# Kernel tuning notes

Hardware: AMD Instinct MI355X
Metric: run time of the kernel (lower is better)

## Reference

```python
import jax, jax.numpy as jnp
import numpy as np

N_OBJ, N_REL = 16384, 32768
HID, POOL = 512, 4096
N_OBJ_CLS, N_REL_CLS = 151, 51


def setup_inputs() -> dict:
    key = jax.random.key(0)
    ks = jax.random.split(key, 12)
    return {
        "edge_ctx": jax.random.normal(ks[0], (N_OBJ, HID), jnp.float32),
        "union_features": jax.random.normal(ks[1], (N_REL, POOL), jnp.float32),
        "pair_idx": jax.random.randint(ks[2], (N_REL, 2), 0, N_OBJ, jnp.int64) if jax.config.jax_enable_x64 else jax.random.randint(ks[2], (N_REL, 2), 0, N_OBJ, jnp.int32),
        "obj_preds": jax.random.randint(ks[3], (N_OBJ,), 0, N_OBJ_CLS, jnp.int32),
        "W_post_emb": jax.random.normal(ks[4], (2 * HID, HID), jnp.float32) * (10.0 / np.sqrt(HID)),
        "b_post_emb": jax.random.normal(ks[5], (2 * HID,), jnp.float32) * 0.01,
        "W_post_cat": jax.random.normal(ks[6], (POOL, 2 * HID), jnp.float32) * (1.0 / np.sqrt(2 * HID)),
        "b_post_cat": jax.random.normal(ks[7], (POOL,), jnp.float32) * 0.01,
        "W_rel": jax.random.normal(ks[8], (N_REL_CLS, POOL), jnp.float32) * (1.0 / np.sqrt(POOL)),
        "b_rel": jax.random.normal(ks[9], (N_REL_CLS,), jnp.float32) * 0.01,
        "freq_bias": jax.random.normal(ks[10], (N_OBJ_CLS, N_OBJ_CLS, N_REL_CLS), jnp.float32),
    }


def reference(edge_ctx, union_features, pair_idx, obj_preds,
              W_post_emb, b_post_emb, W_post_cat, b_post_cat,
              W_rel, b_rel, freq_bias):
    # post_emb: [N_obj, H] -> [N_obj, 2H] -> head/tail reps [N_obj, H]
    edge_rep = edge_ctx @ W_post_emb.T + b_post_emb            # [N_obj, 2H]
    edge_rep = edge_rep.reshape(edge_rep.shape[0], 2, HID)
    head_rep = edge_rep[:, 0]                                  # [N_obj, H]
    tail_rep = edge_rep[:, 1]                                  # [N_obj, H]

    h_idx = pair_idx[:, 0]
    t_idx = pair_idx[:, 1]
    # gather + concat head/tail pair features -> [N_rel, 2H]
    prod_rep = jnp.concatenate([head_rep[h_idx], tail_rep[t_idx]], axis=-1)
    # post_cat linear -> [N_rel, POOL]
    prod_rep = prod_rep @ W_post_cat.T + b_post_cat
    # use_vision, pooling_dim == MLP_HEAD_DIM -> elementwise product
    prod_rep = prod_rep * union_features
    # rel_compress -> [N_rel, num_rel_cls]
    rel_dists = prod_rep @ W_rel.T + b_rel
    # frequency bias lookup indexed by (head class, tail class)
    bias = freq_bias[obj_preds[h_idx], obj_preds[t_idx]]       # [N_rel, num_rel_cls]
    return rel_dists + bias
```

## Files before the change

### kernel.cpp

```cpp
#include <hip/hip_runtime.h>

#define N_OBJ 16384
#define N_REL 32768
#define HID 512
#define POOL 4096
#define NCLS 151
#define NRELCLS 51

#define AS1 __attribute__((address_space(1)))
#define AS3 __attribute__((address_space(3)))

#define LDSSZ 131072

typedef __attribute__((ext_vector_type(8))) short short8;
typedef __attribute__((ext_vector_type(4))) float f32x4;

__device__ __forceinline__ unsigned short f2bf(float x) {
    unsigned u = __float_as_uint(x);
    u += 0x7fff + ((u >> 16) & 1);
    return (unsigned short)(u >> 16);
}

__global__ void cvt_kernel(const float* __restrict__ in, unsigned short* __restrict__ out, long n8) {
    long i = (long)blockIdx.x * blockDim.x + threadIdx.x;
    if (i >= n8) return;
    const float4* p = (const float4*)in;
    float4 a = p[2 * i], b = p[2 * i + 1];
    short8 o;
    o[0] = f2bf(a.x); o[1] = f2bf(a.y); o[2] = f2bf(a.z); o[3] = f2bf(a.w);
    o[4] = f2bf(b.x); o[5] = f2bf(b.y); o[6] = f2bf(b.z); o[7] = f2bf(b.w);
    ((short8*)out)[i] = o;
}

__global__ void cvt_wrel_kernel(const float* __restrict__ W, unsigned short* __restrict__ out) {
    int gid = blockIdx.x * 256 + threadIdx.x;
    int row = gid >> 9;
    int c8 = (gid & 511) << 3;
    short8 o = {};
    if (row < NRELCLS) {
        const float* src = W + (long)row * POOL + c8;
        float4 a = *(const float4*)src, b = *(const float4*)(src + 4);
        o[0] = f2bf(a.x); o[1] = f2bf(a.y); o[2] = f2bf(a.z); o[3] = f2bf(a.w);
        o[4] = f2bf(b.x); o[5] = f2bf(b.y); o[6] = f2bf(b.z); o[7] = f2bf(b.w);
    }
    *(short8*)(out + (long)row * POOL + c8) = o;
}

__device__ __forceinline__ void stage_tile128x64(const unsigned short* __restrict__ src,
                                                 unsigned short* lds,
                                                 int row0, int rowStrideElems, int col0,
                                                 int wave, int lane) {
    const char* s = (const char*)(src + (long)row0 * rowStrideElems + col0);
    long strideB = (long)rowStrideElems * 2;
#pragma unroll
    for (int is = 0; is < 4; ++is) {
        int issue = wave * 4 + is;
        const char* g = s + (long)(issue * 8 + (lane >> 3)) * strideB + (lane & 7) * 16;
        __builtin_amdgcn_global_load_lds((const AS1 void*)g,
                                         (AS3 void*)((char*)lds + issue * 1024),
                                         16, 0, 0);
    }
}

__global__ __launch_bounds__(256) void gemm1_kernel(const unsigned short* __restrict__ A,
                                                    const unsigned short* __restrict__ B,
                                                    const float* __restrict__ bias,
                                                    unsigned short* __restrict__ C) {
    __shared__ __align__(16) unsigned short At[128 * 64];
    __shared__ __align__(16) unsigned short Bt[128 * 64];
    int row0 = blockIdx.x * 128, col0 = blockIdx.y * 128;
    int tid = threadIdx.x, wave = tid >> 6, lane = tid & 63;
    int wr = (wave >> 1) * 64, wc = (wave & 1) * 64;
    int lrow = lane & 15, lko = (lane >> 4) * 8;
    f32x4 acc[4][4] = {};
    for (int kt = 0; kt < HID / 64; ++kt) {
        stage_tile128x64(A, At, row0, HID, kt * 64, wave, lane);
        stage_tile128x64(B, Bt, col0, HID, kt * 64, wave, lane);
        __syncthreads();
#pragma unroll
        for (int ks = 0; ks < 2; ++ks) {
            short8 af[4], bf[4];
#pragma unroll
            for (int mi = 0; mi < 4; ++mi) af[mi] = *(const short8*)(At + (wr + 16 * mi + lrow) * 64 + ks * 32 + lko);
#pragma unroll
            for (int ni = 0; ni < 4; ++ni) bf[ni] = *(const short8*)(Bt + (wc + 16 * ni + lrow) * 64 + ks * 32 + lko);
#pragma unroll
            for (int mi = 0; mi < 4; ++mi)
#pragma unroll
                for (int ni = 0; ni < 4; ++ni)
                    acc[mi][ni] = __builtin_amdgcn_mfma_f32_16x16x32_bf16(af[mi], bf[ni], acc[mi][ni], 0, 0, 0);
        }
        __syncthreads();
    }
#pragma unroll
    for (int mi = 0; mi < 4; ++mi)
#pragma unroll
        for (int ni = 0; ni < 4; ++ni)
#pragma unroll
            for (int i = 0; i < 4; ++i) {
                int r = row0 + wr + 16 * mi + 4 * (lane >> 4) + i;
                int c = col0 + wc + 16 * ni + lrow;
                C[(long)r * 1024 + c] = f2bf(acc[mi][ni][i] + bias[c]);
            }
}

__global__ void init_out_kernel(const int* __restrict__ pair_idx, const int* __restrict__ obj_preds,
                                const float* __restrict__ b_rel, const float* __restrict__ freq_bias,
                                float* __restrict__ out) {
    int r = blockIdx.x * 4 + (threadIdx.x >> 6);
    int lane = threadIdx.x & 63;
    if (lane < NRELCLS) {
        int h = pair_idx[2 * r], t = pair_idx[2 * r + 1];
        long idx = ((long)obj_preds[h] * NCLS + obj_preds[t]) * NRELCLS + lane;
        out[(long)r * NRELCLS + lane] = b_rel[lane] + freq_bias[idx];
    }
}

__device__ __forceinline__ void stage_ab(const char* __restrict__ erepb, const char* __restrict__ Wcb,
                                         char* lds, int s, int t, int col0,
                                         const int* hA, const int* tA, const int* colbA,
                                         const int* obaseA, int w, int lane) {
    int kb = t * 64;
#pragma unroll
    for (int i = 0; i < 2; ++i) {
        int idx = (kb < 1024) ? hA[i] : tA[i];
        __builtin_amdgcn_global_load_lds((const AS1 void*)(erepb + (long)idx * 2048 + kb + colbA[i]),
                                         (AS3 void*)(lds + s * 16384 + obaseA[i]), 16, 0, 0);
        int o = obaseA[i] + lane * 16;
        int row = o >> 6, cin = o & 63;
        int c = cin ^ ((row & 3) << 4);
        __builtin_amdgcn_global_load_lds((const AS1 void*)(Wcb + (long)(col0 + row) * 2048 + kb + c),
                                         (AS3 void*)(lds + 65536 + s * 16384 + obaseA[i]), 16, 0, 0);
    }
}

__device__ __forceinline__ void kstep(const char* lds, int s, int wr, int wc, int lrow, int lcb,
                                      f32x4 acc[8][4]) {
    const char* A = lds + s * 16384;
    const char* B = lds + 65536 + s * 16384;
    short8 bfr[4];
#pragma unroll
    for (int ni = 0; ni < 4; ++ni) {
        int r = wc + 16 * ni + lrow;
        bfr[ni] = *(const short8*)(B + r * 64 + (lcb ^ ((r & 3) << 4)));
    }
    __builtin_amdgcn_s_setprio(1);
#pragma unroll
    for (int mi = 0; mi < 8; ++mi) {
        int r = wr + 16 * mi + lrow;
        short8 a = *(const short8*)(A + r * 64 + (lcb ^ ((r & 3) << 4)));
#pragma unroll
        for (int ni = 0; ni < 4; ++ni)
            acc[mi][ni] = __builtin_amdgcn_mfma_f32_16x16x32_bf16(a, bfr[ni], acc[mi][ni], 0, 0, 0);
    }
    __builtin_amdgcn_s_setprio(0);
}

__global__ __launch_bounds__(512, 1) void fused_kernel(
    const unsigned short* __restrict__ erep,
    const unsigned short* __restrict__ Wcat,
    const unsigned short* __restrict__ Wrelp,
    const float* __restrict__ unionf,
    const float* __restrict__ bcat,
    const int* __restrict__ pair_idx,
    float* __restrict__ out) {
    __shared__ __align__(16) char lds[LDSSZ];
    int bid = blockIdx.x;
    int xcd = bid & 7, j = bid >> 3;
    int panel = (xcd << 1) | (j >> 7);
    int row0 = (j & 127) * 256, col0 = panel * 256;
    int tid = threadIdx.x, w = tid >> 6, lane = tid & 63;
    int wr = (w >> 2) * 128, wc = (w & 3) * 64;
    int lrow = lane & 15, lcb = (lane >> 4) * 16;
    const char* erepb = (const char*)erep;
    const char* Wcb = (const char*)Wcat;
    f32x4 acc2[8][4] = {};

    int hA[2], tA[2], colbA[2], obaseA[2];
#pragma unroll
    for (int i = 0; i < 2; ++i) {
        obaseA[i] = i * 8192 + w * 1024;
        int o = obaseA[i] + lane * 16;
        int arow = o >> 6, cin = o & 63;
        colbA[i] = cin ^ ((arow & 3) << 4);
        hA[i] = pair_idx[2 * (row0 + arow)];
        tA[i] = pair_idx[2 * (row0 + arow) + 1];
    }

    stage_ab(erepb, Wcb, lds, 0, 0, col0, hA, tA, colbA, obaseA, w, lane);
    stage_ab(erepb, Wcb, lds, 1, 1, col0, hA, tA, colbA, obaseA, w, lane);
    stage_ab(erepb, Wcb, lds, 2, 2, col0, hA, tA, colbA, obaseA, w, lane);

    for (int t = 0; t < 30; ++t) {
        asm volatile("s_waitcnt vmcnt(8)" ::: "memory");
        __builtin_amdgcn_s_barrier();
        __builtin_amdgcn_sched_barrier(0);
        if (t < 29) stage_ab(erepb, Wcb, lds, (t + 3) & 3, t + 3, col0, hA, tA, colbA, obaseA, w, lane);
        kstep(lds, t & 3, wr, wc, lrow, lcb, acc2);
    }
    asm volatile("s_waitcnt vmcnt(4)" ::: "memory");
    __builtin_amdgcn_s_barrier();
    __builtin_amdgcn_sched_barrier(0);
    kstep(lds, 30 & 3, wr, wc, lrow, lcb, acc2);
    asm volatile("s_waitcnt vmcnt(0)" ::: "memory");
    __builtin_amdgcn_s_barrier();
    __builtin_amdgcn_sched_barrier(0);
    kstep(lds, 31 & 3, wr, wc, lrow, lcb, acc2);

    asm volatile("s_waitcnt lgkmcnt(0)" ::: "memory");
    __builtin_amdgcn_sched_barrier(0);
    __builtin_amdgcn_s_barrier();
    __builtin_amdgcn_sched_barrier(0);

    {
        float bcv[4];
#pragma unroll
        for (int ni = 0; ni < 4; ++ni) bcv[ni] = bcat[col0 + wc + 16 * ni + lrow];
#pragma unroll
        for (int mi = 0; mi < 8; ++mi)
#pragma unroll
            for (int ni = 0; ni < 4; ++ni) {
                int pcol = wc + 16 * ni + lrow;
#pragma unroll
                for (int i = 0; i < 4; ++i) {
                    int prow = wr + 16 * mi + 4 * (lane >> 4) + i;
                    float u = __builtin_nontemporal_load(
                        &unionf[(long)(row0 + prow) * 4096 + col0 + pcol]);
                    *(unsigned short*)(lds + prow * 512 + ((pcol * 2) ^ ((prow & 7) << 4)))
                        = f2bf((acc2[mi][ni][i] + bcv[ni]) * u);
                }
            }
    }
    asm volatile("s_waitcnt lgkmcnt(0)" ::: "memory");
    __builtin_amdgcn_sched_barrier(0);
    __builtin_amdgcn_s_barrier();
    __builtin_amdgcn_sched_barrier(0);

    f32x4 acc3[2][4] = {};
    const char* Wrb = (const char*)Wrelp;
#pragma unroll
    for (int ks = 0; ks < 8; ++ks) {
        int cb2 = ks * 64 + lcb;
        short8 wb[4], pa[2];
#pragma unroll
        for (int ni = 0; ni < 4; ++ni) {
            int r2 = 16 * ni + lrow;
            wb[ni] = *(const short8*)(Wrb + (long)r2 * 8192 + col0 * 2 + cb2);
        }
#pragma unroll
        for (int mi = 0; mi < 2; ++mi) {
            int r2 = w * 32 + 16 * mi + lrow;
            pa[mi] = *(const short8*)(lds + r2 * 512 + (cb2 ^ ((r2 & 7) << 4)));
        }
#pragma unroll
        for (int mi = 0; mi < 2; ++mi)
#pragma unroll
            for (int ni = 0; ni < 4; ++ni)
                acc3[mi][ni] = __builtin_amdgcn_mfma_f32_16x16x32_bf16(pa[mi], wb[ni], acc3[mi][ni], 0, 0, 0);
    }
#pragma unroll
    for (int mi = 0; mi < 2; ++mi)
#pragma unroll
        for (int ni = 0; ni < 4; ++ni)
#pragma unroll
            for (int i = 0; i < 4; ++i) {
                int r = row0 + w * 32 + 16 * mi + 4 * (lane >> 4) + i;
                int cc = 16 * ni + lrow;
                if (cc < NRELCLS) atomicAdd(out + (long)r * NRELCLS + cc, acc3[mi][ni][i]);
            }
}

extern "C" void kernel_launch(void* const* d_in, const int* in_sizes, int n_in,
                              void* d_out, int out_size, void* d_ws, size_t ws_size,
                              hipStream_t stream) {
    const float* edge_ctx  = (const float*)d_in[0];
    const float* unionf    = (const float*)d_in[1];
    const int*   pair_idx  = (const int*)d_in[2];
    const int*   obj_preds = (const int*)d_in[3];
    const float* W_emb     = (const float*)d_in[4];
    const float* b_emb     = (const float*)d_in[5];
    const float* W_cat     = (const float*)d_in[6];
    const float* b_cat     = (const float*)d_in[7];
    const float* W_rel     = (const float*)d_in[8];
    const float* b_rel     = (const float*)d_in[9];
    const float* freq_bias = (const float*)d_in[10];
    float* out = (float*)d_out;

    char* ws = (char*)d_ws;
    unsigned short* ecb   = (unsigned short*)ws; ws += (size_t)N_OBJ * HID * 2;
    unsigned short* Wembb = (unsigned short*)ws; ws += (size_t)1024 * HID * 2;
    unsigned short* Wcatb = (unsigned short*)ws; ws += (size_t)POOL * 1024 * 2;
    unsigned short* Wrelb = (unsigned short*)ws; ws += (size_t)64 * POOL * 2;
    unsigned short* erep  = (unsigned short*)ws; ws += (size_t)N_OBJ * 1024 * 2;

    cvt_kernel<<<4096, 256, 0, stream>>>(edge_ctx, ecb, (long)N_OBJ * HID / 8);
    cvt_kernel<<<256, 256, 0, stream>>>(W_emb, Wembb, (long)1024 * HID / 8);
    cvt_kernel<<<2048, 256, 0, stream>>>(W_cat, Wcatb, (long)POOL * 1024 / 8);
    cvt_wrel_kernel<<<128, 256, 0, stream>>>(W_rel, Wrelb);
    gemm1_kernel<<<dim3(128, 8), 256, 0, stream>>>(ecb, Wembb, b_emb, erep);
    init_out_kernel<<<8192, 256, 0, stream>>>(pair_idx, obj_preds, b_rel, freq_bias, out);
    fused_kernel<<<2048, 512, 0, stream>>>(erep, Wcatb, Wrelb, unionf, b_cat, pair_idx, out);
}
```

Before: 552.0 us.

## Switch GEMM mainloop to double-buffered 128-wide K tiles with interleaved staging

Changes the post_cat GEMM mainloop from a 4-stage ring of 64-byte K slices to 2 LDS buffers of 128-byte K slices, cutting the iteration count from 32 to 16. The loads for the next tile are issued in two halves, interleaved with four sub-phases of MFMA work, and the swizzle is widened to 8 rows. The aim is fewer barriers per unit of compute and finer overlap of loads with MFMAs. The cost is a shallower prefetch depth and extra barriers inside each iteration, which may expose load latency for the gathered rows.

```diff
diff --git a/kernel.cpp b/kernel.cpp
--- a/kernel.cpp
+++ b/kernel.cpp
@@ -116,43 +116,52 @@
     }
 }
 
-__device__ __forceinline__ void stage_ab(const char* __restrict__ erepb, const char* __restrict__ Wcb,
-                                         char* lds, int s, int t, int col0,
-                                         const int* hA, const int* tA, const int* colbA,
-                                         const int* obaseA, int w, int lane) {
-    int kb = t * 64;
-#pragma unroll
-    for (int i = 0; i < 2; ++i) {
-        int idx = (kb < 1024) ? hA[i] : tA[i];
+__device__ __forceinline__ void stage_half(const char* __restrict__ erepb, const char* __restrict__ Wcb,
+                                           char* lds, int slot, int t, int i0, int col0,
+                                           const int* hA, const int* tA,
+                                           const int* arowA, const int* colbA, int w) {
+    int kb = t * 128;
+    int head = (kb < 1024);
+#pragma unroll
+    for (int i = i0; i < i0 + 2; ++i) {
+        int obase = i * 8192 + w * 1024;
+        int idx = head ? hA[i] : tA[i];
         __builtin_amdgcn_global_load_lds((const AS1 void*)(erepb + (long)idx * 2048 + kb + colbA[i]),
-                                         (AS3 void*)(lds + s * 16384 + obaseA[i]), 16, 0, 0);
-        int o = obaseA[i] + lane * 16;
-        int row = o >> 6, cin = o & 63;
-        int c = cin ^ ((row & 3) << 4);
-        __builtin_amdgcn_global_load_lds((const AS1 void*)(Wcb + (long)(col0 + row) * 2048 + kb + c),
-                                         (AS3 void*)(lds + 65536 + s * 16384 + obaseA[i]), 16, 0, 0);
-    }
-}
-
-__device__ __forceinline__ void kstep(const char* lds, int s, int wr, int wc, int lrow, int lcb,
-                                      f32x4 acc[8][4]) {
-    const char* A = lds + s * 16384;
-    const char* B = lds + 65536 + s * 16384;
-    short8 bfr[4];
-#pragma unroll
-    for (int ni = 0; ni < 4; ++ni) {
-        int r = wc + 16 * ni + lrow;
-        bfr[ni] = *(const short8*)(B + r * 64 + (lcb ^ ((r & 3) << 4)));
-    }
+                                         (AS3 void*)(lds + slot * 32768 + obase), 16, 0, 0);
+        __builtin_amdgcn_global_load_lds((const AS1 void*)(Wcb + (long)(col0 + arowA[i]) * 2048 + kb + colbA[i]),
+                                         (AS3 void*)(lds + 65536 + slot * 32768 + obase), 16, 0, 0);
+    }
+}
+
+__device__ __forceinline__ void read_bfrags(const char* B, int wc, int lrow, int lcb, short8 bF[4][2]) {
+#pragma unroll
+    for (int ni = 0; ni < 4; ++ni)
+#pragma unroll
+        for (int ks = 0; ks < 2; ++ks) {
+            int r = wc + 16 * ni + lrow;
+            bF[ni][ks] = *(const short8*)(B + r * 128 + ((ks * 64 + lcb) ^ ((r & 7) << 4)));
+        }
+}
+
+__device__ __forceinline__ void read_afrags(const char* A, int p, int wr, int lrow, int lcb, short8 aF[2][2]) {
+#pragma unroll
+    for (int m = 0; m < 2; ++m)
+#pragma unroll
+        for (int ks = 0; ks < 2; ++ks) {
+            int r = wr + 16 * (2 * p + m) + lrow;
+            aF[m][ks] = *(const short8*)(A + r * 128 + ((ks * 64 + lcb) ^ ((r & 7) << 4)));
+        }
+}
+
+__device__ __forceinline__ void mfma16(int p, short8 aF[2][2], short8 bF[4][2], f32x4 acc[8][4]) {
     __builtin_amdgcn_s_setprio(1);
 #pragma unroll
-    for (int mi = 0; mi < 8; ++mi) {
-        int r = wr + 16 * mi + lrow;
-        short8 a = *(const short8*)(A + r * 64 + (lcb ^ ((r & 3) << 4)));
+    for (int m = 0; m < 2; ++m)
 #pragma unroll
         for (int ni = 0; ni < 4; ++ni)
-            acc[mi][ni] = __builtin_amdgcn_mfma_f32_16x16x32_bf16(a, bfr[ni], acc[mi][ni], 0, 0, 0);
-    }
+#pragma unroll
+            for (int ks = 0; ks < 2; ++ks)
+                acc[2 * p + m][ni] = __builtin_amdgcn_mfma_f32_16x16x32_bf16(aF[m][ks], bF[ni][ks], acc[2 * p + m][ni], 0, 0, 0);
     __builtin_amdgcn_s_setprio(0);
 }
 
@@ -176,36 +185,52 @@
     const char* Wcb = (const char*)Wcat;
     f32x4 acc2[8][4] = {};
 
-    int hA[2], tA[2], colbA[2], obaseA[2];
-#pragma unroll
-    for (int i = 0; i < 2; ++i) {
-        obaseA[i] = i * 8192 + w * 1024;
-        int o = obaseA[i] + lane * 16;
-        int arow = o >> 6, cin = o & 63;
-        colbA[i] = cin ^ ((arow & 3) << 4);
-        hA[i] = pair_idx[2 * (row0 + arow)];
-        tA[i] = pair_idx[2 * (row0 + arow) + 1];
-    }
-
-    stage_ab(erepb, Wcb, lds, 0, 0, col0, hA, tA, colbA, obaseA, w, lane);
-    stage_ab(erepb, Wcb, lds, 1, 1, col0, hA, tA, colbA, obaseA, w, lane);
-    stage_ab(erepb, Wcb, lds, 2, 2, col0, hA, tA, colbA, obaseA, w, lane);
-
-    for (int t = 0; t < 30; ++t) {
-        asm volatile("s_waitcnt vmcnt(8)" ::: "memory");
-        __builtin_amdgcn_s_barrier();
-        __builtin_amdgcn_sched_barrier(0);
-        if (t < 29) stage_ab(erepb, Wcb, lds, (t + 3) & 3, t + 3, col0, hA, tA, colbA, obaseA, w, lane);
-        kstep(lds, t & 3, wr, wc, lrow, lcb, acc2);
-    }
-    asm volatile("s_waitcnt vmcnt(4)" ::: "memory");
-    __builtin_amdgcn_s_barrier();
-    __builtin_amdgcn_sched_barrier(0);
-    kstep(lds, 30 & 3, wr, wc, lrow, lcb, acc2);
-    asm volatile("s_waitcnt vmcnt(0)" ::: "memory");
-    __builtin_amdgcn_s_barrier();
-    __builtin_amdgcn_sched_barrier(0);
-    kstep(lds, 31 & 3, wr, wc, lrow, lcb, acc2);
+    int hA[4], tA[4], arowA[4], colbA[4];
+#pragma unroll
+    for (int i = 0; i < 4; ++i) {
+        int o = i * 8192 + w * 1024 + lane * 16;
+        int ar = o >> 7, cin = o & 127;
+        arowA[i] = ar;
+        colbA[i] = cin ^ ((ar & 7) << 4);
+        hA[i] = pair_idx[2 * (row0 + ar)];
+        tA[i] = pair_idx[2 * (row0 + ar) + 1];
+    }
+
+    stage_half(erepb, Wcb, lds, 0, 0, 0, col0, hA, tA, arowA, colbA, w);
+    stage_half(erepb, Wcb, lds, 0, 0, 2, col0, hA, tA, arowA, colbA, w);
+
+    for (int t = 0; t < 16; ++t) {
+        const char* A = lds + (t & 1) * 32768;
+        const char* B = lds + 65536 + (t & 1) * 32768;
+        int sn = (t + 1) & 1;
+        short8 bF[4][2];
+#pragma unroll
+        for (int p = 0; p < 4; ++p) {
+            short8 aF[2][2];
+            if (p == 0) {
+                if (t < 15) {
+                    stage_half(erepb, Wcb, lds, sn, t + 1, 0, col0, hA, tA, arowA, colbA, w);
+                    asm volatile("s_waitcnt vmcnt(4)" ::: "memory");
+                } else {
+                    asm volatile("s_waitcnt vmcnt(0)" ::: "memory");
+                }
+                __builtin_amdgcn_s_barrier();
+                __builtin_amdgcn_sched_barrier(0);
+                read_bfrags(B, wc, lrow, lcb, bF);
+                read_afrags(A, 0, wr, lrow, lcb, aF);
+            } else {
+                read_afrags(A, p, wr, lrow, lcb, aF);
+                if (p == 2 && t < 15)
+                    stage_half(erepb, Wcb, lds, sn, t + 1, 2, col0, hA, tA, arowA, colbA, w);
+                __builtin_amdgcn_s_barrier();
+                __builtin_amdgcn_sched_barrier(0);
+            }
+            asm volatile("s_waitcnt lgkmcnt(0)" ::: "memory");
+            __builtin_amdgcn_sched_barrier(0);
+            mfma16(p, aF, bF, acc2);
+            __builtin_amdgcn_s_barrier();
+        }
+    }
 
     asm volatile("s_waitcnt lgkmcnt(0)" ::: "memory");
     __builtin_amdgcn_sched_barrier(0);
```

New measurement: 519.3 us. 1.06x faster.
